# Optimization experiments

Measured on AMD Instinct MI355X. Metric: run time of the kernel, lower is better.

Reference implementation:

```python
import jax, jax.numpy as jnp
import numpy as np

NUM_ITEMS = 20000
NUM_ENTITIES = 60000
NUM_RELATIONS = 24
D = 128
E = 32
ALPHA = 0.2      # LeakyReLU slope
MASK_VAL = -9e15


def setup_inputs() -> dict:
    key = jax.random.key(0)
    ks = jax.random.split(key, 12)
    inp = {
        'emb_item0':   jax.random.normal(ks[0], (NUM_ITEMS, D), jnp.float32) * 0.1,
        'emb_item1':   jax.random.normal(ks[1], (NUM_ITEMS, D), jnp.float32) * 0.1,
        'emb_entity0': jax.random.normal(ks[2], (NUM_ENTITIES + 1, D), jnp.float32) * 0.1,
        'emb_entity1': jax.random.normal(ks[3], (NUM_ENTITIES + 1, D), jnp.float32) * 0.1,
        'emb_rel0':    jax.random.normal(ks[4], (NUM_RELATIONS + 1, D), jnp.float32) * 0.1,
        'emb_rel1':    jax.random.normal(ks[5], (NUM_RELATIONS + 1, D), jnp.float32) * 0.1,
        'fc_w':        jax.random.normal(ks[6], (3 * D,), jnp.float32) * 0.05,
        'fc_b':        jax.random.normal(ks[7], (1,), jnp.float32) * 0.05,
        'out_w':       jax.random.normal(ks[8], (D, D), jnp.float32) * 0.05,
        'out_b':       jax.random.normal(ks[9], (D,), jnp.float32) * 0.05,
        'item_entities':  jax.random.randint(ks[10], (NUM_ITEMS, E), 0, NUM_ENTITIES + 1, jnp.int64 if jax.config.jax_enable_x64 else jnp.int32),
        'item_relations': jax.random.randint(ks[11], (NUM_ITEMS, E), 0, NUM_RELATIONS + 1, jnp.int64 if jax.config.jax_enable_x64 else jnp.int32),
    }
    return inp


def _gat_forward_relation(item_embs, ent_embs, rel_embs, mask, fc_w, fc_b, out_w, out_b):
    # fc(cat([Wh, rel, We])) with Wh broadcast of item_embs; split the 3D weight
    w_h, w_r, w_e = fc_w[:D], fc_w[D:2 * D], fc_w[2 * D:]
    e = (item_embs @ w_h)[:, None] \
        + jnp.einsum('ned,d->ne', rel_embs, w_r) \
        + jnp.einsum('ned,d->ne', ent_embs, w_e) + fc_b[0]     # [N, E]
    e = jnp.where(e > 0, e, ALPHA * e)                          # LeakyReLU
    e = jnp.where(mask > 0, e, MASK_VAL)                        # adjacency mask
    att = jax.nn.softmax(e, axis=1)                             # [N, E]
    h = jnp.einsum('ne,ned->nd', att, ent_embs)                 # bmm aggregate
    x = (h + item_embs) @ out_w + out_b                         # out Linear
    return jnp.maximum(x, 0.0)                                  # ReLU


def reference(emb_item0, emb_item1, emb_entity0, emb_entity1, emb_rel0, emb_rel1,
              fc_w, fc_b, out_w, out_b, item_entities, item_relations):
    mask = (item_entities != NUM_ENTITIES).astype(jnp.float32)  # padding mask
    items0 = _gat_forward_relation(emb_item0, emb_entity0[item_entities],
                                   emb_rel0[item_relations], mask,
                                   fc_w, fc_b, out_w, out_b)
    items1 = _gat_forward_relation(emb_item1, emb_entity1[item_entities],
                                   emb_rel1[item_relations], mask,
                                   fc_w, fc_b, out_w, out_b)
    return (items0 + items1) * 0.5
```

## Files before the change

kernel.cpp:

```cpp
#include <hip/hip_runtime.h>

#define NI 20000
#define NET 60001
#define MASKED_ID 60000
#define NRT 25
#define MASK_VAL -9000000000000000.0f

#define OFF_RELDOT0 0
#define OFF_RELDOT1 32
#define OFF_IHB0   64
#define OFF_IHB1   (64 + 20000)
#define OFF_EDOT0  (64 + 40000)
#define OFF_EDOT1  (64 + 40000 + 60004)
#define OFF_G1     160128

__global__ __launch_bounds__(256) void dots_kernel(
    const float* __restrict__ it0, const float* __restrict__ it1,
    const float* __restrict__ en0, const float* __restrict__ en1,
    const float* __restrict__ re0, const float* __restrict__ re1,
    const float* __restrict__ fcw, const float* __restrict__ fcb,
    float* __restrict__ ws)
{
    const float* tbl; const float* w; float* out; int n; float bm;
    switch (blockIdx.y) {
      case 0:  tbl = en0; w = fcw + 256; out = ws + OFF_EDOT0;   n = NET; bm = 0.f; break;
      case 1:  tbl = en1; w = fcw + 256; out = ws + OFF_EDOT1;   n = NET; bm = 0.f; break;
      case 2:  tbl = it0; w = fcw;       out = ws + OFF_IHB0;    n = NI;  bm = 1.f; break;
      case 3:  tbl = it1; w = fcw;       out = ws + OFF_IHB1;    n = NI;  bm = 1.f; break;
      case 4:  tbl = re0; w = fcw + 128; out = ws + OFF_RELDOT0; n = NRT; bm = 0.f; break;
      default: tbl = re1; w = fcw + 128; out = ws + OFF_RELDOT1; n = NRT; bm = 0.f; break;
    }
    const int tid = blockIdx.x * 256 + threadIdx.x;
    const int row = tid >> 3;
    const int sub = tid & 7;
    if (row >= n) return;
    const float4* trow = (const float4*)(tbl + (size_t)row * 128) + sub * 4;
    const float4* wv   = (const float4*)(w) + sub * 4;
    float d = 0.f;
    #pragma unroll
    for (int q = 0; q < 4; ++q) {
        float4 a = trow[q]; float4 b = wv[q];
        d += a.x * b.x + a.y * b.y + a.z * b.z + a.w * b.w;
    }
    d += __shfl_xor(d, 1);
    d += __shfl_xor(d, 2);
    d += __shfl_xor(d, 4);
    if (sub == 0) out[row] = d + bm * fcb[0];
}

__global__ __launch_bounds__(256) void attn_kernel(
    const float2* __restrict__ it0, const float2* __restrict__ it1,
    const float2* __restrict__ en0, const float2* __restrict__ en1,
    const int* __restrict__ idx_e, const int* __restrict__ idx_r,
    const float* __restrict__ ws, float2* __restrict__ g0, float2* __restrict__ g1)
{
    const int p = blockIdx.y;
    const float2* ent  = p ? en1 : en0;
    const float2* itm  = p ? it1 : it0;
    const float* edot  = ws + (p ? OFF_EDOT1 : OFF_EDOT0);
    const float* ihb   = ws + (p ? OFF_IHB1  : OFF_IHB0);
    const float* rdot  = ws + (p ? OFF_RELDOT1 : OFF_RELDOT0);
    float2* g = p ? g1 : g0;

    const int lane = threadIdx.x & 63;
    const int n = blockIdx.x * 4 + (threadIdx.x >> 6);
    const int k = lane & 31;

    const int ide = idx_e[n * 32 + k];
    const int idr = idx_r[n * 32 + k];
    float e = ihb[n] + rdot[idr] + edot[ide];
    e = e > 0.f ? e : 0.2f * e;
    if (ide == MASKED_ID) e = MASK_VAL;

    float m = e;
    #pragma unroll
    for (int msk = 1; msk < 32; msk <<= 1) m = fmaxf(m, __shfl_xor(m, msk));
    const float ex = __expf(e - m);
    float s = ex;
    #pragma unroll
    for (int msk = 1; msk < 32; msk <<= 1) s += __shfl_xor(s, msk);
    const float att = ex / s;

    float2 h = make_float2(0.f, 0.f);
    #pragma unroll
    for (int kk = 0; kk < 32; ++kk) {
        const float a = __shfl(att, kk);
        const int  id = __shfl(ide, kk);
        const float2 v = ent[id * 64 + lane];
        h.x = fmaf(a, v.x, h.x);
        h.y = fmaf(a, v.y, h.y);
    }
    const float2 t = itm[n * 64 + lane];
    g[n * 64 + lane] = make_float2(h.x + t.x, h.y + t.y);
}

__global__ __launch_bounds__(256) void out_kernel(
    const float2* __restrict__ g0, const float2* __restrict__ g1,
    const float* __restrict__ W, const float* __restrict__ ob,
    float2* __restrict__ out)
{
    __shared__ float2 Ws[64][64];
    __shared__ float  gs[2][16][128];

    const int tid = threadIdx.x;
    const int j   = tid & 63;
    const int wv  = tid >> 6;
    const int nb  = blockIdx.x * 16;

    {
        const float4* s0 = (const float4*)g0;
        const float4* s1 = (const float4*)g1;
        #pragma unroll
        for (int r = 0; r < 4; ++r) {
            const int q = r * 256 + tid;
            const int path = q >> 9;
            const int it   = (q >> 5) & 15;
            const int c    = q & 31;
            const float4* src = path ? s1 : s0;
            ((float4*)gs)[q] = src[(nb + it) * 32 + c];
        }
    }

    float2 acc[2][4];
    #pragma unroll
    for (int pp = 0; pp < 2; ++pp)
        #pragma unroll
        for (int t = 0; t < 4; ++t) acc[pp][t] = make_float2(0.f, 0.f);

    const int ib = wv * 4;
    for (int half = 0; half < 2; ++half) {
        __syncthreads();
        const float2* Wsrc = (const float2*)(W + half * 64 * 128);
        #pragma unroll
        for (int r = 0; r < 16; ++r) {
            const int q = r * 256 + tid;
            ((float2*)Ws)[q] = Wsrc[q];
        }
        __syncthreads();

        #pragma unroll 4
        for (int i4 = 0; i4 < 16; ++i4) {
            const int i = i4 * 4;
            const float2 w0 = Ws[i][j],   w1 = Ws[i+1][j];
            const float2 w2 = Ws[i+2][j], w3 = Ws[i+3][j];
            #pragma unroll
            for (int t = 0; t < 4; ++t) {
                const float4 a0 = *(const float4*)&gs[0][ib + t][half * 64 + i];
                const float4 a1 = *(const float4*)&gs[1][ib + t][half * 64 + i];
                acc[0][t].x = fmaf(a0.x, w0.x, acc[0][t].x);
                acc[0][t].x = fmaf(a0.y, w1.x, acc[0][t].x);
                acc[0][t].x = fmaf(a0.z, w2.x, acc[0][t].x);
                acc[0][t].x = fmaf(a0.w, w3.x, acc[0][t].x);
                acc[0][t].y = fmaf(a0.x, w0.y, acc[0][t].y);
                acc[0][t].y = fmaf(a0.y, w1.y, acc[0][t].y);
                acc[0][t].y = fmaf(a0.z, w2.y, acc[0][t].y);
                acc[0][t].y = fmaf(a0.w, w3.y, acc[0][t].y);
                acc[1][t].x = fmaf(a1.x, w0.x, acc[1][t].x);
                acc[1][t].x = fmaf(a1.y, w1.x, acc[1][t].x);
                acc[1][t].x = fmaf(a1.z, w2.x, acc[1][t].x);
                acc[1][t].x = fmaf(a1.w, w3.x, acc[1][t].x);
                acc[1][t].y = fmaf(a1.x, w0.y, acc[1][t].y);
                acc[1][t].y = fmaf(a1.y, w1.y, acc[1][t].y);
                acc[1][t].y = fmaf(a1.z, w2.y, acc[1][t].y);
                acc[1][t].y = fmaf(a1.w, w3.y, acc[1][t].y);
            }
        }
    }

    const float2 b = ((const float2*)ob)[j];
    #pragma unroll
    for (int t = 0; t < 4; ++t) {
        const int n = nb + ib + t;
        const float r0x = fmaxf(acc[0][t].x + b.x, 0.f);
        const float r0y = fmaxf(acc[0][t].y + b.y, 0.f);
        const float r1x = fmaxf(acc[1][t].x + b.x, 0.f);
        const float r1y = fmaxf(acc[1][t].y + b.y, 0.f);
        out[n * 64 + j] = make_float2(0.5f * (r0x + r1x), 0.5f * (r0y + r1y));
    }
}

extern "C" void kernel_launch(void* const* d_in, const int* in_sizes, int n_in,
                              void* d_out, int out_size, void* d_ws, size_t ws_size,
                              hipStream_t stream)
{
    const float* it0 = (const float*)d_in[0];
    const float* it1 = (const float*)d_in[1];
    const float* en0 = (const float*)d_in[2];
    const float* en1 = (const float*)d_in[3];
    const float* re0 = (const float*)d_in[4];
    const float* re1 = (const float*)d_in[5];
    const float* fcw = (const float*)d_in[6];
    const float* fcb = (const float*)d_in[7];
    const float* ow  = (const float*)d_in[8];
    const float* obv = (const float*)d_in[9];
    const int* ie    = (const int*)d_in[10];
    const int* ir    = (const int*)d_in[11];

    float* ws  = (float*)d_ws;
    float* g0  = (float*)d_out;
    float* g1  = ws + OFF_G1;

    dim3 gp((NET * 8 + 255) / 256, 6);
    hipLaunchKernelGGL(dots_kernel, gp, dim3(256), 0, stream,
                       it0, it1, en0, en1, re0, re1, fcw, fcb, ws);

    dim3 ga(NI / 4, 2);
    hipLaunchKernelGGL(attn_kernel, ga, dim3(256), 0, stream,
                       (const float2*)it0, (const float2*)it1,
                       (const float2*)en0, (const float2*)en1,
                       ie, ir, ws, (float2*)g0, (float2*)g1);

    hipLaunchKernelGGL(out_kernel, dim3(NI / 16), dim3(256), 0, stream,
                       (const float2*)g0, (const float2*)g1, ow, obv,
                       (float2*)d_out);
}
```

Before: 235.3 us.

## Process both paths per wave with float4 gathers and prefetched entity rows

The attention kernel now handles both embedding paths for an item in one wave, with each 32-lane half serving one path and loading float4 entity rows instead of float2. The first 16 entity rows are issued into registers before the softmax so gather latency overlaps the reduction, and the second 16 are loaded while the first batch is accumulated. Index and score loads are shared across both paths, and the grid drops its path dimension. The 16-entry float4 prefetch buffer raises register pressure, and launch bounds of 3 constrain allocation, which may cause spills.

```diff
diff --git a/kernel.cpp b/kernel.cpp
--- a/kernel.cpp
+++ b/kernel.cpp
@@ -48,30 +48,40 @@
     if (sub == 0) out[row] = d + bm * fcb[0];
 }
 
-__global__ __launch_bounds__(256) void attn_kernel(
-    const float2* __restrict__ it0, const float2* __restrict__ it1,
-    const float2* __restrict__ en0, const float2* __restrict__ en1,
+__global__ __launch_bounds__(256, 3) void attn_kernel(
+    const float4* __restrict__ it0, const float4* __restrict__ it1,
+    const float4* __restrict__ en0, const float4* __restrict__ en1,
     const int* __restrict__ idx_e, const int* __restrict__ idx_r,
-    const float* __restrict__ ws, float2* __restrict__ g0, float2* __restrict__ g1)
-{
-    const int p = blockIdx.y;
-    const float2* ent  = p ? en1 : en0;
-    const float2* itm  = p ? it1 : it0;
-    const float* edot  = ws + (p ? OFF_EDOT1 : OFF_EDOT0);
-    const float* ihb   = ws + (p ? OFF_IHB1  : OFF_IHB0);
-    const float* rdot  = ws + (p ? OFF_RELDOT1 : OFF_RELDOT0);
-    float2* g = p ? g1 : g0;
-
+    const float* __restrict__ ws, float4* __restrict__ g0, float4* __restrict__ g1)
+{
     const int lane = threadIdx.x & 63;
-    const int n = blockIdx.x * 4 + (threadIdx.x >> 6);
-    const int k = lane & 31;
+    const int half = lane >> 5;
+    const int k    = lane & 31;
+    const int n    = blockIdx.x * 4 + (threadIdx.x >> 6);
+
+    const float4* entv = half ? en1 : en0;
+    const float4* itmv = half ? it1 : it0;
+    const float* edot  = ws + (half ? OFF_EDOT1 : OFF_EDOT0);
+    const float* ihb   = ws + (half ? OFF_IHB1  : OFF_IHB0);
+    const float* rdot  = ws + (half ? OFF_RELDOT1 : OFF_RELDOT0);
 
     const int ide = idx_e[n * 32 + k];
     const int idr = idx_r[n * 32 + k];
-    float e = ihb[n] + rdot[idr] + edot[ide];
+    const float epart = ihb[n] + rdot[idr];
+    const float ed = edot[ide];
+
+    float4 vb[16];
+    #pragma unroll
+    for (int kk = 0; kk < 16; ++kk) {
+        const int idA = __shfl(ide, kk);
+        const int idB = __shfl(ide, kk + 32);
+        const int id  = half ? idB : idA;
+        vb[kk] = entv[id * 32 + k];
+    }
+
+    float e = epart + ed;
     e = e > 0.f ? e : 0.2f * e;
     if (ide == MASKED_ID) e = MASK_VAL;
-
     float m = e;
     #pragma unroll
     for (int msk = 1; msk < 32; msk <<= 1) m = fmaxf(m, __shfl_xor(m, msk));
@@ -81,17 +91,36 @@
     for (int msk = 1; msk < 32; msk <<= 1) s += __shfl_xor(s, msk);
     const float att = ex / s;
 
-    float2 h = make_float2(0.f, 0.f);
-    #pragma unroll
-    for (int kk = 0; kk < 32; ++kk) {
-        const float a = __shfl(att, kk);
-        const int  id = __shfl(ide, kk);
-        const float2 v = ent[id * 64 + lane];
-        h.x = fmaf(a, v.x, h.x);
-        h.y = fmaf(a, v.y, h.y);
-    }
-    const float2 t = itm[n * 64 + lane];
-    g[n * 64 + lane] = make_float2(h.x + t.x, h.y + t.y);
+    float4 h = make_float4(0.f, 0.f, 0.f, 0.f);
+    #pragma unroll
+    for (int kk = 0; kk < 16; ++kk) {
+        const int idA = __shfl(ide, kk + 16);
+        const int idB = __shfl(ide, kk + 48);
+        const int id  = half ? idB : idA;
+        const float4 vn = entv[id * 32 + k];
+        const float aA = __shfl(att, kk);
+        const float aB = __shfl(att, kk + 32);
+        const float a  = half ? aB : aA;
+        h.x = fmaf(a, vb[kk].x, h.x);
+        h.y = fmaf(a, vb[kk].y, h.y);
+        h.z = fmaf(a, vb[kk].z, h.z);
+        h.w = fmaf(a, vb[kk].w, h.w);
+        vb[kk] = vn;
+    }
+    #pragma unroll
+    for (int kk = 0; kk < 16; ++kk) {
+        const float aA = __shfl(att, kk + 16);
+        const float aB = __shfl(att, kk + 48);
+        const float a  = half ? aB : aA;
+        h.x = fmaf(a, vb[kk].x, h.x);
+        h.y = fmaf(a, vb[kk].y, h.y);
+        h.z = fmaf(a, vb[kk].z, h.z);
+        h.w = fmaf(a, vb[kk].w, h.w);
+    }
+
+    const float4 t = itmv[n * 32 + k];
+    float4* g = half ? g1 : g0;
+    g[n * 32 + k] = make_float4(h.x + t.x, h.y + t.y, h.z + t.z, h.w + t.w);
 }
 
 __global__ __launch_bounds__(256) void out_kernel(
@@ -204,11 +233,10 @@
     hipLaunchKernelGGL(dots_kernel, gp, dim3(256), 0, stream,
                        it0, it1, en0, en1, re0, re1, fcw, fcb, ws);
 
-    dim3 ga(NI / 4, 2);
-    hipLaunchKernelGGL(attn_kernel, ga, dim3(256), 0, stream,
-                       (const float2*)it0, (const float2*)it1,
-                       (const float2*)en0, (const float2*)en1,
-                       ie, ir, ws, (float2*)g0, (float2*)g1);
+    hipLaunchKernelGGL(attn_kernel, dim3(NI / 4), dim3(256), 0, stream,
+                       (const float4*)it0, (const float4*)it1,
+                       (const float4*)en0, (const float4*)en1,
+                       ie, ir, ws, (float4*)g0, (float4*)g1);
 
     hipLaunchKernelGGL(out_kernel, dim3(NI / 16), dim3(256), 0, stream,
                        (const float2*)g0, (const float2*)g1, ow, obv,
```

After: 247.4 us. 5.1% more time.

## Gather bf16-packed entity embeddings in attention aggregation

Applied to the files above, without the earlier changes.

The dots kernel now also writes a bf16 copy of both entity tables into workspace, interleaved per row. The attention kernel gathers these packed values instead of fp32 rows, halving the bytes moved by the random gather. This adds a conversion write each call, lowers precision of the aggregated features, and is enabled only when the workspace is large enough.

```diff
diff --git a/kernel.cpp b/kernel.cpp
--- a/kernel.cpp
+++ b/kernel.cpp
@@ -13,13 +13,23 @@
 #define OFF_EDOT0  (64 + 40000)
 #define OFF_EDOT1  (64 + 40000 + 60004)
 #define OFF_G1     160128
+#define OFF_ENTB   2720256
+#define WS_NEED_BYTES ((size_t)(OFF_ENTB + (size_t)60004 * 128) * 4ull)
+
+__device__ __forceinline__ unsigned pack_bf16x2(float x, float y) {
+    unsigned bx = __builtin_bit_cast(unsigned, x);
+    unsigned by = __builtin_bit_cast(unsigned, y);
+    bx = bx + 0x7fffu + ((bx >> 16) & 1u);
+    by = by + 0x7fffu + ((by >> 16) & 1u);
+    return (bx >> 16) | (by & 0xffff0000u);
+}
 
 __global__ __launch_bounds__(256) void dots_kernel(
     const float* __restrict__ it0, const float* __restrict__ it1,
     const float* __restrict__ en0, const float* __restrict__ en1,
     const float* __restrict__ re0, const float* __restrict__ re1,
     const float* __restrict__ fcw, const float* __restrict__ fcb,
-    float* __restrict__ ws)
+    float* __restrict__ ws, int writeB)
 {
     const float* tbl; const float* w; float* out; int n; float bm;
     switch (blockIdx.y) {
@@ -36,18 +46,34 @@
     if (row >= n) return;
     const float4* trow = (const float4*)(tbl + (size_t)row * 128) + sub * 4;
     const float4* wv   = (const float4*)(w) + sub * 4;
+    float4 a0 = trow[0], a1 = trow[1], a2 = trow[2], a3 = trow[3];
     float d = 0.f;
-    #pragma unroll
-    for (int q = 0; q < 4; ++q) {
-        float4 a = trow[q]; float4 b = wv[q];
-        d += a.x * b.x + a.y * b.y + a.z * b.z + a.w * b.w;
+    {
+        float4 b;
+        b = wv[0]; d += a0.x*b.x + a0.y*b.y + a0.z*b.z + a0.w*b.w;
+        b = wv[1]; d += a1.x*b.x + a1.y*b.y + a1.z*b.z + a1.w*b.w;
+        b = wv[2]; d += a2.x*b.x + a2.y*b.y + a2.z*b.z + a2.w*b.w;
+        b = wv[3]; d += a3.x*b.x + a3.y*b.y + a3.z*b.z + a3.w*b.w;
     }
     d += __shfl_xor(d, 1);
     d += __shfl_xor(d, 2);
     d += __shfl_xor(d, 4);
     if (sub == 0) out[row] = d + bm * fcb[0];
-}
-
+
+    if (writeB && blockIdx.y < 2) {
+        const int p = blockIdx.y;
+        uint4* eb = (uint4*)((unsigned*)(ws + OFF_ENTB)
+                             + (size_t)row * 128 + p * 64 + sub * 8);
+        uint4 w0, w1;
+        w0.x = pack_bf16x2(a0.x, a0.y); w0.y = pack_bf16x2(a0.z, a0.w);
+        w0.z = pack_bf16x2(a1.x, a1.y); w0.w = pack_bf16x2(a1.z, a1.w);
+        w1.x = pack_bf16x2(a2.x, a2.y); w1.y = pack_bf16x2(a2.z, a2.w);
+        w1.z = pack_bf16x2(a3.x, a3.y); w1.w = pack_bf16x2(a3.z, a3.w);
+        eb[0] = w0; eb[1] = w1;
+    }
+}
+
+template<int BF16>
 __global__ __launch_bounds__(256) void attn_kernel(
     const float2* __restrict__ it0, const float2* __restrict__ it1,
     const float2* __restrict__ en0, const float2* __restrict__ en1,
@@ -81,17 +107,31 @@
     for (int msk = 1; msk < 32; msk <<= 1) s += __shfl_xor(s, msk);
     const float att = ex / s;
 
-    float2 h = make_float2(0.f, 0.f);
-    #pragma unroll
-    for (int kk = 0; kk < 32; ++kk) {
-        const float a = __shfl(att, kk);
-        const int  id = __shfl(ide, kk);
-        const float2 v = ent[id * 64 + lane];
-        h.x = fmaf(a, v.x, h.x);
-        h.y = fmaf(a, v.y, h.y);
+    float hx = 0.f, hy = 0.f;
+    if (BF16) {
+        const unsigned* entB = (const unsigned*)(ws + OFF_ENTB) + p * 64 + lane;
+        #pragma unroll
+        for (int kk = 0; kk < 32; ++kk) {
+            const float a = __shfl(att, kk);
+            const int  id = __shfl(ide, kk);
+            const unsigned wbits = entB[(size_t)id * 128];
+            const float vx = __builtin_bit_cast(float, wbits << 16);
+            const float vy = __builtin_bit_cast(float, wbits & 0xffff0000u);
+            hx = fmaf(a, vx, hx);
+            hy = fmaf(a, vy, hy);
+        }
+    } else {
+        #pragma unroll
+        for (int kk = 0; kk < 32; ++kk) {
+            const float a = __shfl(att, kk);
+            const int  id = __shfl(ide, kk);
+            const float2 v = ent[id * 64 + lane];
+            hx = fmaf(a, v.x, hx);
+            hy = fmaf(a, v.y, hy);
+        }
     }
     const float2 t = itm[n * 64 + lane];
-    g[n * 64 + lane] = make_float2(h.x + t.x, h.y + t.y);
+    g[n * 64 + lane] = make_float2(hx + t.x, hy + t.y);
 }
 
 __global__ __launch_bounds__(256) void out_kernel(
@@ -200,15 +240,23 @@
     float* g0  = (float*)d_out;
     float* g1  = ws + OFF_G1;
 
+    const int useB = (ws_size >= WS_NEED_BYTES) ? 1 : 0;
+
     dim3 gp((NET * 8 + 255) / 256, 6);
     hipLaunchKernelGGL(dots_kernel, gp, dim3(256), 0, stream,
-                       it0, it1, en0, en1, re0, re1, fcw, fcb, ws);
+                       it0, it1, en0, en1, re0, re1, fcw, fcb, ws, useB);
 
     dim3 ga(NI / 4, 2);
-    hipLaunchKernelGGL(attn_kernel, ga, dim3(256), 0, stream,
-                       (const float2*)it0, (const float2*)it1,
-                       (const float2*)en0, (const float2*)en1,
-                       ie, ir, ws, (float2*)g0, (float2*)g1);
+    if (useB)
+        hipLaunchKernelGGL((attn_kernel<1>), ga, dim3(256), 0, stream,
+                           (const float2*)it0, (const float2*)it1,
+                           (const float2*)en0, (const float2*)en1,
+                           ie, ir, ws, (float2*)g0, (float2*)g1);
+    else
+        hipLaunchKernelGGL((attn_kernel<0>), ga, dim3(256), 0, stream,
+                           (const float2*)it0, (const float2*)it1,
+                           (const float2*)en0, (const float2*)en1,
+                           ie, ir, ws, (float2*)g0, (float2*)g1);
 
     hipLaunchKernelGGL(out_kernel, dim3(NI / 16), dim3(256), 0, stream,
                        (const float2*)g0, (const float2*)g1, ow, obv,
```

New measurement: 201.4 us. 14.4% less time.
